# Optimization experiments

Hardware: AMD Instinct MI355X
Metric: run time of the kernel (lower is better)

## Reference

```python
import jax, jax.numpy as jnp
import numpy as np
import math

BBOX_XFORM_CLIP = math.log(1000.0 / 16.0)  # standard BoxCoder clip on dw/dh
WX, WY, WW, WH = 10.0, 10.0, 5.0, 5.0      # BoxCoder weights
TO_REMOVE = 1.0                             # legacy +1 box convention


def _decode(rel_codes, boxes):
    # boxes: [N,4] xyxy reference proposals; rel_codes: [N,4] deltas
    widths = boxes[:, 2] - boxes[:, 0] + TO_REMOVE
    heights = boxes[:, 3] - boxes[:, 1] + TO_REMOVE
    ctr_x = boxes[:, 0] + 0.5 * widths
    ctr_y = boxes[:, 1] + 0.5 * heights

    dx = rel_codes[:, 0] / WX
    dy = rel_codes[:, 1] / WY
    dw = jnp.minimum(rel_codes[:, 2] / WW, BBOX_XFORM_CLIP)
    dh = jnp.minimum(rel_codes[:, 3] / WH, BBOX_XFORM_CLIP)

    pred_ctr_x = dx * widths + ctr_x
    pred_ctr_y = dy * heights + ctr_y
    pred_w = jnp.exp(dw) * widths
    pred_h = jnp.exp(dh) * heights

    x1 = pred_ctr_x - 0.5 * pred_w
    y1 = pred_ctr_y - 0.5 * pred_h
    x2 = pred_ctr_x + 0.5 * pred_w - 1.0
    y2 = pred_ctr_y + 0.5 * pred_h - 1.0
    return jnp.stack([x1, y1, x2, y2], axis=1)


def setup_inputs() -> dict:
    key = jax.random.key(0)
    k1, k2, k3, k4 = jax.random.split(key, 4)
    N, C = 262144, 81
    W = H = 1024
    class_logits = jax.random.normal(k1, (N, C), dtype=jnp.float32)
    box_regression = jax.random.normal(k2, (N, 4), dtype=jnp.float32) * 0.5
    # valid xyxy proposals inside the image: x2 > x1, y2 > y1
    xy1 = jax.random.uniform(k3, (N, 2), dtype=jnp.float32) * (W - 64.0)
    wh = jax.random.uniform(k4, (N, 2), dtype=jnp.float32) * 60.0 + 2.0
    proposal_boxes = jnp.concatenate([xy1, xy1 + wh], axis=1)
    return {
        "class_logits": class_logits,
        "box_regression": box_regression,
        "proposal_boxes": proposal_boxes,
        "img_w": W,
        "img_h": H,
    }


def reference(class_logits, box_regression, proposal_boxes, img_w, img_h):
    # softmax over classes
    class_prob = jax.nn.softmax(class_logits, axis=-1)  # [N, C]
    rel = box_regression[:, -4:]
    proposals = _decode(rel, proposal_boxes)            # [N, 4]
    proposals = jnp.maximum(proposals, 0.0)             # proposals[proposals < 0] = 0
    C = class_prob.shape[1]
    # is_repeat path: repeat decoded box for every class, then per-row boxlist
    boxes = jnp.tile(proposals, (1, C)).reshape(-1, 4)  # [N*C, 4]
    # clip_to_image (remove_empty=False): clamp to [0, W-1] x [0, H-1]
    wmax = jnp.asarray(img_w - 1, dtype=boxes.dtype)
    hmax = jnp.asarray(img_h - 1, dtype=boxes.dtype)
    x1 = jnp.clip(boxes[:, 0], 0.0, wmax)
    y1 = jnp.clip(boxes[:, 1], 0.0, hmax)
    x2 = jnp.clip(boxes[:, 2], 0.0, wmax)
    y2 = jnp.clip(boxes[:, 3], 0.0, hmax)
    boxes = jnp.stack([x1, y1, x2, y2], axis=1)         # [N*C, 4]
    scores = class_prob.reshape(-1)                     # [N*C]
    return boxes, scores
```

## Files before the change

kernel.cpp:

```cpp
#include <hip/hip_runtime.h>
#include <math.h>

#define NUM_CLASSES 81
#define WAVES_PER_BLOCK 4

__global__ __launch_bounds__(256) void postproc_kernel(
    const float* __restrict__ logits,
    const float* __restrict__ box_reg,
    const float* __restrict__ prop,
    const int* __restrict__ img_w_p,
    const int* __restrict__ img_h_p,
    float* __restrict__ out_boxes,
    float* __restrict__ out_scores,
    int N)
{
    const int wave = threadIdx.x >> 6;
    const int lane = threadIdx.x & 63;
    const int row  = blockIdx.x * WAVES_PER_BLOCK + wave;
    if (row >= N) return;

    const float wmax = (float)(*img_w_p) - 1.0f;
    const float hmax = (float)(*img_h_p) - 1.0f;

    const float b0 = prop[row * 4 + 0];
    const float b1 = prop[row * 4 + 1];
    const float b2 = prop[row * 4 + 2];
    const float b3 = prop[row * 4 + 3];
    const float r0 = box_reg[row * 4 + 0];
    const float r1 = box_reg[row * 4 + 1];
    const float r2 = box_reg[row * 4 + 2];
    const float r3 = box_reg[row * 4 + 3];

    const float BBOX_XFORM_CLIP = 4.135166556742356f;
    const float w  = b2 - b0 + 1.0f;
    const float h  = b3 - b1 + 1.0f;
    const float cx = b0 + 0.5f * w;
    const float cy = b1 + 0.5f * h;
    const float dx = r0 / 10.0f;
    const float dy = r1 / 10.0f;
    const float dw = fminf(r2 / 5.0f, BBOX_XFORM_CLIP);
    const float dh = fminf(r3 / 5.0f, BBOX_XFORM_CLIP);
    const float px = dx * w + cx;
    const float py = dy * h + cy;
    const float pw = expf(dw) * w;
    const float ph = expf(dh) * h;
    const float x1 = fminf(fmaxf(px - 0.5f * pw, 0.0f), wmax);
    const float y1 = fminf(fmaxf(py - 0.5f * ph, 0.0f), hmax);
    const float x2 = fminf(fmaxf(px + 0.5f * pw - 1.0f, 0.0f), wmax);
    const float y2 = fminf(fmaxf(py + 0.5f * ph - 1.0f, 0.0f), hmax);
    const float4 box = make_float4(x1, y1, x2, y2);

    const float* lrow = logits + (size_t)row * NUM_CLASSES;
    const bool has2 = (lane < NUM_CLASSES - 64);
    float v0 = lrow[lane];
    float v1 = has2 ? lrow[64 + lane] : -INFINITY;

    float m = fmaxf(v0, v1);
    #pragma unroll
    for (int off = 32; off > 0; off >>= 1)
        m = fmaxf(m, __shfl_xor(m, off));

    float e0 = expf(v0 - m);
    float e1 = has2 ? expf(v1 - m) : 0.0f;
    float s = e0 + e1;
    #pragma unroll
    for (int off = 32; off > 0; off >>= 1)
        s += __shfl_xor(s, off);

    float4* brow = reinterpret_cast<float4*>(out_boxes + (size_t)row * (NUM_CLASSES * 4));
    float*  srow = out_scores + (size_t)row * NUM_CLASSES;

    brow[lane] = box;
    srow[lane] = e0 / s;
    if (has2) {
        brow[64 + lane] = box;
        srow[64 + lane] = e1 / s;
    }
}

extern "C" void kernel_launch(void* const* d_in, const int* in_sizes, int n_in,
                              void* d_out, int out_size, void* d_ws, size_t ws_size,
                              hipStream_t stream) {
    const float* logits  = (const float*)d_in[0];
    const float* box_reg = (const float*)d_in[1];
    const float* prop    = (const float*)d_in[2];
    const int*   img_w_p = (const int*)d_in[3];
    const int*   img_h_p = (const int*)d_in[4];

    const int N = in_sizes[1] / 4;

    float* out_boxes  = (float*)d_out;
    float* out_scores = out_boxes + (size_t)N * NUM_CLASSES * 4;

    const int blocks = (N + WAVES_PER_BLOCK - 1) / WAVES_PER_BLOCK;
    postproc_kernel<<<blocks, 256, 0, stream>>>(
        logits, box_reg, prop, img_w_p, img_h_p, out_boxes, out_scores, N);
}
```

Before: 500.3 us.

## Split softmax postprocess into per-row stats kernel and flat coalesced write kernel

```diff
diff --git a/kernel.cpp b/kernel.cpp
--- a/kernel.cpp
+++ b/kernel.cpp
@@ -2,53 +2,21 @@
 #include <math.h>
 
 #define NUM_CLASSES 81
-#define WAVES_PER_BLOCK 4
 
-__global__ __launch_bounds__(256) void postproc_kernel(
+__global__ __launch_bounds__(256) void stats_kernel(
     const float* __restrict__ logits,
     const float* __restrict__ box_reg,
     const float* __restrict__ prop,
     const int* __restrict__ img_w_p,
     const int* __restrict__ img_h_p,
-    float* __restrict__ out_boxes,
-    float* __restrict__ out_scores,
+    float4* __restrict__ ws_box,
+    float2* __restrict__ ws_ms,
     int N)
 {
     const int wave = threadIdx.x >> 6;
     const int lane = threadIdx.x & 63;
-    const int row  = blockIdx.x * WAVES_PER_BLOCK + wave;
+    const int row  = blockIdx.x * 4 + wave;
     if (row >= N) return;
-
-    const float wmax = (float)(*img_w_p) - 1.0f;
-    const float hmax = (float)(*img_h_p) - 1.0f;
-
-    const float b0 = prop[row * 4 + 0];
-    const float b1 = prop[row * 4 + 1];
-    const float b2 = prop[row * 4 + 2];
-    const float b3 = prop[row * 4 + 3];
-    const float r0 = box_reg[row * 4 + 0];
-    const float r1 = box_reg[row * 4 + 1];
-    const float r2 = box_reg[row * 4 + 2];
-    const float r3 = box_reg[row * 4 + 3];
-
-    const float BBOX_XFORM_CLIP = 4.135166556742356f;
-    const float w  = b2 - b0 + 1.0f;
-    const float h  = b3 - b1 + 1.0f;
-    const float cx = b0 + 0.5f * w;
-    const float cy = b1 + 0.5f * h;
-    const float dx = r0 / 10.0f;
-    const float dy = r1 / 10.0f;
-    const float dw = fminf(r2 / 5.0f, BBOX_XFORM_CLIP);
-    const float dh = fminf(r3 / 5.0f, BBOX_XFORM_CLIP);
-    const float px = dx * w + cx;
-    const float py = dy * h + cy;
-    const float pw = expf(dw) * w;
-    const float ph = expf(dh) * h;
-    const float x1 = fminf(fmaxf(px - 0.5f * pw, 0.0f), wmax);
-    const float y1 = fminf(fmaxf(py - 0.5f * ph, 0.0f), hmax);
-    const float x2 = fminf(fmaxf(px + 0.5f * pw - 1.0f, 0.0f), wmax);
-    const float y2 = fminf(fmaxf(py + 0.5f * ph - 1.0f, 0.0f), hmax);
-    const float4 box = make_float4(x1, y1, x2, y2);
 
     const float* lrow = logits + (size_t)row * NUM_CLASSES;
     const bool has2 = (lane < NUM_CLASSES - 64);
@@ -60,22 +28,62 @@
     for (int off = 32; off > 0; off >>= 1)
         m = fmaxf(m, __shfl_xor(m, off));
 
-    float e0 = expf(v0 - m);
-    float e1 = has2 ? expf(v1 - m) : 0.0f;
-    float s = e0 + e1;
+    float s = expf(v0 - m) + (has2 ? expf(v1 - m) : 0.0f);
     #pragma unroll
     for (int off = 32; off > 0; off >>= 1)
         s += __shfl_xor(s, off);
 
-    float4* brow = reinterpret_cast<float4*>(out_boxes + (size_t)row * (NUM_CLASSES * 4));
-    float*  srow = out_scores + (size_t)row * NUM_CLASSES;
+    if (lane == 0) {
+        const float wmax = (float)(*img_w_p) - 1.0f;
+        const float hmax = (float)(*img_h_p) - 1.0f;
+        const float b0 = prop[row * 4 + 0];
+        const float b1 = prop[row * 4 + 1];
+        const float b2 = prop[row * 4 + 2];
+        const float b3 = prop[row * 4 + 3];
+        const float r0 = box_reg[row * 4 + 0];
+        const float r1 = box_reg[row * 4 + 1];
+        const float r2 = box_reg[row * 4 + 2];
+        const float r3 = box_reg[row * 4 + 3];
 
-    brow[lane] = box;
-    srow[lane] = e0 / s;
-    if (has2) {
-        brow[64 + lane] = box;
-        srow[64 + lane] = e1 / s;
+        const float BBOX_XFORM_CLIP = 4.135166556742356f;
+        const float w  = b2 - b0 + 1.0f;
+        const float h  = b3 - b1 + 1.0f;
+        const float cx = b0 + 0.5f * w;
+        const float cy = b1 + 0.5f * h;
+        const float dx = r0 * 0.1f;
+        const float dy = r1 * 0.1f;
+        const float dw = fminf(r2 * 0.2f, BBOX_XFORM_CLIP);
+        const float dh = fminf(r3 * 0.2f, BBOX_XFORM_CLIP);
+        const float px = dx * w + cx;
+        const float py = dy * h + cy;
+        const float pw = expf(dw) * w;
+        const float ph = expf(dh) * h;
+        const float x1 = fminf(fmaxf(px - 0.5f * pw, 0.0f), wmax);
+        const float y1 = fminf(fmaxf(py - 0.5f * ph, 0.0f), hmax);
+        const float x2 = fminf(fmaxf(px + 0.5f * pw - 1.0f, 0.0f), wmax);
+        const float y2 = fminf(fmaxf(py + 0.5f * ph - 1.0f, 0.0f), hmax);
+
+        ws_box[row] = make_float4(x1, y1, x2, y2);
+        ws_ms[row]  = make_float2(m, 1.0f / s);
     }
+}
+
+__global__ __launch_bounds__(256) void write_kernel(
+    const float* __restrict__ logits,
+    const float4* __restrict__ ws_box,
+    const float2* __restrict__ ws_ms,
+    float4* __restrict__ out_boxes,
+    float* __restrict__ out_scores,
+    int total)
+{
+    const int j = blockIdx.x * blockDim.x + threadIdx.x;
+    if (j >= total) return;
+    const unsigned row = (unsigned)j / (unsigned)NUM_CLASSES;
+    const float4 box = ws_box[row];
+    const float2 ms  = ws_ms[row];
+    const float  sc  = __expf(logits[j] - ms.x) * ms.y;
+    out_boxes[j]  = box;
+    out_scores[j] = sc;
 }
 
 extern "C" void kernel_launch(void* const* d_in, const int* in_sizes, int n_in,
@@ -88,11 +96,19 @@
     const int*   img_h_p = (const int*)d_in[4];
 
     const int N = in_sizes[1] / 4;
+    const int total = N * NUM_CLASSES;
 
     float* out_boxes  = (float*)d_out;
     float* out_scores = out_boxes + (size_t)N * NUM_CLASSES * 4;
 
-    const int blocks = (N + WAVES_PER_BLOCK - 1) / WAVES_PER_BLOCK;
-    postproc_kernel<<<blocks, 256, 0, stream>>>(
-        logits, box_reg, prop, img_w_p, img_h_p, out_boxes, out_scores, N);
+    float4* ws_box = (float4*)d_ws;
+    float2* ws_ms  = (float2*)((char*)d_ws + (size_t)N * sizeof(float4));
+
+    const int blocks1 = (N + 3) / 4;
+    stats_kernel<<<blocks1, 256, 0, stream>>>(
+        logits, box_reg, prop, img_w_p, img_h_p, ws_box, ws_ms, N);
+
+    const int blocks2 = (total + 255) / 256;
+    write_kernel<<<blocks2, 256, 0, stream>>>(
+        logits, ws_box, ws_ms, (float4*)out_boxes, out_scores, total);
 }
```

New measurement: 553.0 us. +10.5%, slower.

## Stage block rows in LDS for contiguous coalesced logit loads and output stores

Applied to the files above, without the earlier changes.

```diff
diff --git a/kernel.cpp b/kernel.cpp
--- a/kernel.cpp
+++ b/kernel.cpp
@@ -2,97 +2,134 @@
 #include <math.h>
 
 #define NUM_CLASSES 81
-#define WAVES_PER_BLOCK 4
+#define ROWS_PER_BLOCK 16
+#define ELEMS_PER_BLOCK (ROWS_PER_BLOCK * NUM_CLASSES)
 
-__global__ __launch_bounds__(256) void postproc_kernel(
+__global__ __launch_bounds__(256) void fused_kernel(
     const float* __restrict__ logits,
-    const float* __restrict__ box_reg,
-    const float* __restrict__ prop,
+    const float4* __restrict__ box_reg4,
+    const float4* __restrict__ prop4,
     const int* __restrict__ img_w_p,
     const int* __restrict__ img_h_p,
-    float* __restrict__ out_boxes,
+    float4* __restrict__ out_boxes4,
     float* __restrict__ out_scores,
     int N)
 {
-    const int wave = threadIdx.x >> 6;
-    const int lane = threadIdx.x & 63;
-    const int row  = blockIdx.x * WAVES_PER_BLOCK + wave;
-    if (row >= N) return;
+    __shared__ float  lds_val[ELEMS_PER_BLOCK];
+    __shared__ float4 lds_box[ROWS_PER_BLOCK];
 
-    const float wmax = (float)(*img_w_p) - 1.0f;
-    const float hmax = (float)(*img_h_p) - 1.0f;
+    const int tid = threadIdx.x;
+    const int block_row0 = blockIdx.x * ROWS_PER_BLOCK;
+    if (block_row0 >= N) return;
+    const int rows  = min(ROWS_PER_BLOCK, N - block_row0);
+    const int elems = rows * NUM_CLASSES;
 
-    const float b0 = prop[row * 4 + 0];
-    const float b1 = prop[row * 4 + 1];
-    const float b2 = prop[row * 4 + 2];
-    const float b3 = prop[row * 4 + 3];
-    const float r0 = box_reg[row * 4 + 0];
-    const float r1 = box_reg[row * 4 + 1];
-    const float r2 = box_reg[row * 4 + 2];
-    const float r3 = box_reg[row * 4 + 3];
+    const float* lbase = logits + (size_t)block_row0 * NUM_CLASSES;
+    #pragma unroll
+    for (int i = 0; i < 6; ++i) {
+        int e = tid + i * 256;
+        if (e < elems) lds_val[e] = lbase[e];
+    }
 
-    const float BBOX_XFORM_CLIP = 4.135166556742356f;
-    const float w  = b2 - b0 + 1.0f;
-    const float h  = b3 - b1 + 1.0f;
-    const float cx = b0 + 0.5f * w;
-    const float cy = b1 + 0.5f * h;
-    const float dx = r0 / 10.0f;
-    const float dy = r1 / 10.0f;
-    const float dw = fminf(r2 / 5.0f, BBOX_XFORM_CLIP);
-    const float dh = fminf(r3 / 5.0f, BBOX_XFORM_CLIP);
-    const float px = dx * w + cx;
-    const float py = dy * h + cy;
-    const float pw = expf(dw) * w;
-    const float ph = expf(dh) * h;
-    const float x1 = fminf(fmaxf(px - 0.5f * pw, 0.0f), wmax);
-    const float y1 = fminf(fmaxf(py - 0.5f * ph, 0.0f), hmax);
-    const float x2 = fminf(fmaxf(px + 0.5f * pw - 1.0f, 0.0f), wmax);
-    const float y2 = fminf(fmaxf(py + 0.5f * ph - 1.0f, 0.0f), hmax);
-    const float4 box = make_float4(x1, y1, x2, y2);
+    if (tid < rows) {
+        const int row = block_row0 + tid;
+        const float4 b = prop4[row];
+        const float4 r = box_reg4[row];
+        const float wmax = (float)(*img_w_p) - 1.0f;
+        const float hmax = (float)(*img_h_p) - 1.0f;
 
-    const float* lrow = logits + (size_t)row * NUM_CLASSES;
-    const bool has2 = (lane < NUM_CLASSES - 64);
-    float v0 = lrow[lane];
-    float v1 = has2 ? lrow[64 + lane] : -INFINITY;
+        const float BBOX_XFORM_CLIP = 4.135166556742356f;
+        const float w  = b.z - b.x + 1.0f;
+        const float h  = b.w - b.y + 1.0f;
+        const float cx = b.x + 0.5f * w;
+        const float cy = b.y + 0.5f * h;
+        const float dx = r.x * 0.1f;
+        const float dy = r.y * 0.1f;
+        const float dw = fminf(r.z * 0.2f, BBOX_XFORM_CLIP);
+        const float dh = fminf(r.w * 0.2f, BBOX_XFORM_CLIP);
+        const float px = dx * w + cx;
+        const float py = dy * h + cy;
+        const float pw = expf(dw) * w;
+        const float ph = expf(dh) * h;
+        const float x1 = fminf(fmaxf(px - 0.5f * pw, 0.0f), wmax);
+        const float y1 = fminf(fmaxf(py - 0.5f * ph, 0.0f), hmax);
+        const float x2 = fminf(fmaxf(px + 0.5f * pw - 1.0f, 0.0f), wmax);
+        const float y2 = fminf(fmaxf(py + 0.5f * ph - 1.0f, 0.0f), hmax);
+        lds_box[tid] = make_float4(x1, y1, x2, y2);
+    }
+    __syncthreads();
 
-    float m = fmaxf(v0, v1);
+    const int sub = tid & 15;
+    const int rl  = tid >> 4;
+    if (rl < rows) {
+        float* rowv = lds_val + rl * NUM_CLASSES;
+
+        float v[6];
+        float m = -INFINITY;
+        #pragma unroll
+        for (int i = 0; i < 6; ++i) {
+            const int k = sub + i * 16;
+            if (k < NUM_CLASSES) { v[i] = rowv[k]; m = fmaxf(m, v[i]); }
+            else                 { v[i] = -INFINITY; }
+        }
+        #pragma unroll
+        for (int off = 1; off <= 8; off <<= 1)
+            m = fmaxf(m, __shfl_xor(m, off));
+
+        float s = 0.0f;
+        #pragma unroll
+        for (int i = 0; i < 6; ++i) {
+            const int k = sub + i * 16;
+            if (k < NUM_CLASSES) { v[i] = __expf(v[i] - m); s += v[i]; }
+        }
+        #pragma unroll
+        for (int off = 1; off <= 8; off <<= 1)
+            s += __shfl_xor(s, off);
+
+        const float inv = 1.0f / s;
+        #pragma unroll
+        for (int i = 0; i < 6; ++i) {
+            const int k = sub + i * 16;
+            if (k < NUM_CLASSES) rowv[k] = v[i] * inv;
+        }
+    }
+    __syncthreads();
+
+    const size_t sbase = (size_t)block_row0 * NUM_CLASSES;
+
+    float* sdst = out_scores + sbase;
     #pragma unroll
-    for (int off = 32; off > 0; off >>= 1)
-        m = fmaxf(m, __shfl_xor(m, off));
+    for (int i = 0; i < 6; ++i) {
+        int e = tid + i * 256;
+        if (e < elems) sdst[e] = lds_val[e];
+    }
 
-    float e0 = expf(v0 - m);
-    float e1 = has2 ? expf(v1 - m) : 0.0f;
-    float s = e0 + e1;
+    float4* bdst = out_boxes4 + sbase;
     #pragma unroll
-    for (int off = 32; off > 0; off >>= 1)
-        s += __shfl_xor(s, off);
-
-    float4* brow = reinterpret_cast<float4*>(out_boxes + (size_t)row * (NUM_CLASSES * 4));
-    float*  srow = out_scores + (size_t)row * NUM_CLASSES;
-
-    brow[lane] = box;
-    srow[lane] = e0 / s;
-    if (has2) {
-        brow[64 + lane] = box;
-        srow[64 + lane] = e1 / s;
+    for (int i = 0; i < 6; ++i) {
+        int j = tid + i * 256;
+        if (j < elems) {
+            const int r = (int)(((unsigned)j * 12946u) >> 20);
+            bdst[j] = lds_box[r];
+        }
     }
 }
 
 extern "C" void kernel_launch(void* const* d_in, const int* in_sizes, int n_in,
                               void* d_out, int out_size, void* d_ws, size_t ws_size,
                               hipStream_t stream) {
-    const float* logits  = (const float*)d_in[0];
-    const float* box_reg = (const float*)d_in[1];
-    const float* prop    = (const float*)d_in[2];
-    const int*   img_w_p = (const int*)d_in[3];
-    const int*   img_h_p = (const int*)d_in[4];
+    const float* logits   = (const float*)d_in[0];
+    const float4* boxreg4 = (const float4*)d_in[1];
+    const float4* prop4   = (const float4*)d_in[2];
+    const int*   img_w_p  = (const int*)d_in[3];
+    const int*   img_h_p  = (const int*)d_in[4];
 
     const int N = in_sizes[1] / 4;
 
-    float* out_boxes  = (float*)d_out;
-    float* out_scores = out_boxes + (size_t)N * NUM_CLASSES * 4;
+    float4* out_boxes4 = (float4*)d_out;
+    float*  out_scores = (float*)d_out + (size_t)N * NUM_CLASSES * 4;
 
-    const int blocks = (N + WAVES_PER_BLOCK - 1) / WAVES_PER_BLOCK;
-    postproc_kernel<<<blocks, 256, 0, stream>>>(
-        logits, box_reg, prop, img_w_p, img_h_p, out_boxes, out_scores, N);
+    const int blocks = (N + ROWS_PER_BLOCK - 1) / ROWS_PER_BLOCK;
+    fused_kernel<<<blocks, 256, 0, stream>>>(
+        logits, boxreg4, prop4, img_w_p, img_h_p, out_boxes4, out_scores, N);
 }
```

After: 492.2 us. Within noise of the previous version (-1.6%).
